# Performance work log

Hardware: AMD Instinct MI355X
Metric: run time of the kernel (lower is better)

Reference implementation:

```python
import jax, jax.numpy as jnp
import numpy as np

B, S, HID = 2, 1024, 4096
NH, NKV, HD = 32, 8, 128
EPS = 1e-6
ROPE_THETA = 1000000.0
SCALE = HD ** -0.5
NREP = NH // NKV


def _rope_tables(batch, seq, head_dim, theta):
    inv_freq = 1.0 / (theta ** (np.arange(0, head_dim, 2, dtype=np.float32) / head_dim))
    pos = np.arange(seq, dtype=np.float32)
    freqs = np.outer(pos, inv_freq)            # [S, HD/2]
    emb = np.concatenate([freqs, freqs], -1)   # [S, HD]
    cos = np.broadcast_to(np.cos(emb), (batch, seq, head_dim))
    sin = np.broadcast_to(np.sin(emb), (batch, seq, head_dim))
    return jnp.asarray(cos), jnp.asarray(sin)


def setup_inputs() -> dict:
    key = jax.random.key(0)
    k1, k2, k3 = jax.random.split(key, 3)
    hidden_states = jax.random.normal(k1, (B, S, HID), dtype=jnp.float32)
    cos, sin = _rope_tables(B, S, HD, ROPE_THETA)
    attention_mask = jnp.ones((B, 1, S, S), dtype=bool)
    w_qkv = jax.random.normal(k2, ((NH + 2 * NKV) * HD, HID), dtype=jnp.float32) * (HID ** -0.5)
    w_q_norm = jnp.ones((HD,), dtype=jnp.float32)
    w_k_norm = jnp.ones((HD,), dtype=jnp.float32)
    w_o = jax.random.normal(k3, (HID, NH * HD), dtype=jnp.float32) * ((NH * HD) ** -0.5)
    return {"hidden_states": hidden_states, "cos": cos, "sin": sin,
            "attention_mask": attention_mask, "w_qkv": w_qkv,
            "w_q_norm": w_q_norm, "w_k_norm": w_k_norm, "w_o": w_o}


def _rms_norm(x, w):
    var = jnp.mean(jnp.square(x), axis=-1, keepdims=True)
    return x * jax.lax.rsqrt(var + EPS) * w


def _rotate_half(x):
    x1, x2 = jnp.split(x, 2, axis=-1)
    return jnp.concatenate([-x2, x1], axis=-1)


def reference(hidden_states, cos, sin, attention_mask, w_qkv, w_q_norm, w_k_norm, w_o):
    qkv = jnp.einsum('bsh,oh->bso', hidden_states, w_qkv)  # [B,S,(NH+2NKV)*HD]
    q, k, v = jnp.split(qkv, [NH * HD, (NH + NKV) * HD], axis=-1)
    q = _rms_norm(q.reshape(B, S, NH, HD), w_q_norm).transpose(0, 2, 1, 3)   # [B,NH,S,HD]
    k = _rms_norm(k.reshape(B, S, NKV, HD), w_k_norm).transpose(0, 2, 1, 3)  # [B,NKV,S,HD]
    v = v.reshape(B, S, NKV, HD).transpose(0, 2, 1, 3)                        # [B,NKV,S,HD]
    c = cos[:, None, :, :]
    s = sin[:, None, :, :]
    q = q * c + _rotate_half(q) * s
    k = k * c + _rotate_half(k) * s
    k = jnp.repeat(k, NREP, axis=1)  # GQA repeat -> [B,NH,S,HD]
    v = jnp.repeat(v, NREP, axis=1)
    scores = jnp.einsum('bhqd,bhkd->bhqk', q, k) * SCALE
    scores = jnp.where(attention_mask, scores, jnp.finfo(scores.dtype).min)
    attn = jax.nn.softmax(scores, axis=-1)
    out = jnp.einsum('bhqk,bhkd->bhqd', attn, v)
    out = out.transpose(0, 2, 1, 3).reshape(B, S, NH * HD)
    return jnp.einsum('bsd,od->bso', out, w_o)
```

## Files before the change

kernel.cpp:

```cpp
#include <hip/hip_runtime.h>
#include <hip/hip_bf16.h>

typedef __bf16 bf16_t;
typedef bf16_t bf16x2 __attribute__((ext_vector_type(2)));
typedef bf16_t bf16x4 __attribute__((ext_vector_type(4)));
typedef bf16_t bf16x8 __attribute__((ext_vector_type(8)));
typedef float f32x4 __attribute__((ext_vector_type(4)));

#define DEVI __device__ __forceinline__

DEVI void gld_lds16(const void* g, void* l) {
  __builtin_amdgcn_global_load_lds(
      (const __attribute__((address_space(1))) void*)g,
      (__attribute__((address_space(3))) void*)l, 16, 0, 0);
}

__global__ __launch_bounds__(256) void cvt_f32_bf16(
    const float* __restrict__ in, bf16_t* __restrict__ out, long n) {
  long i = ((long)blockIdx.x * 256 + threadIdx.x) * 8;
  if (i >= n) return;
  float4 a = *(const float4*)(in + i);
  float4 b = *(const float4*)(in + i + 4);
  bf16x8 v = {(__bf16)a.x, (__bf16)a.y, (__bf16)a.z, (__bf16)a.w,
              (__bf16)b.x, (__bf16)b.y, (__bf16)b.z, (__bf16)b.w};
  *(bf16x8*)(out + i) = v;
}

__global__ __launch_bounds__(256) void cvt_f32_bf16_2(
    const float* __restrict__ ina, bf16_t* __restrict__ outa, long na,
    const float* __restrict__ inb, bf16_t* __restrict__ outb, long nb) {
  long i = ((long)blockIdx.x * 256 + threadIdx.x) * 8;
  const float* src;
  bf16_t* dst;
  if (i < na) {
    src = ina + i;
    dst = outa + i;
  } else {
    long j = i - na;
    if (j >= nb) return;
    src = inb + j;
    dst = outb + j;
  }
  float4 a = *(const float4*)src;
  float4 b = *(const float4*)(src + 4);
  bf16x8 v = {(__bf16)a.x, (__bf16)a.y, (__bf16)a.z, (__bf16)a.w,
              (__bf16)b.x, (__bf16)b.y, (__bf16)b.z, (__bf16)b.w};
  *(bf16x8*)dst = v;
}

template <int FC, int MINW, typename CT>
__global__ __launch_bounds__(512, MINW) void gemm128(
    const bf16_t* __restrict__ A, const bf16_t* __restrict__ W,
    CT* __restrict__ C, int M, int N, int K) {
  constexpr int BN = FC * 64;
  constexpr int P1 = FC / 2, P2 = FC - P1;
  __shared__ __align__(16) bf16_t As[2][128 * 64];
  __shared__ __align__(16) bf16_t Bs[2][BN * 64];
  const int tid = threadIdx.x, wave = tid >> 6, lane = tid & 63;
  const int q16 = lane & 15, gq = lane >> 4, sw = q16 & 7;
  const int wm = wave >> 2, wn = wave & 3;
  const int nM = M >> 7, nN = N / BN;
  const int cM = nM >> 1, cN = nN >> 2;
  const int xcd = (int)blockIdx.x & 7, wi = (int)blockIdx.x >> 3;
  const int tm = ((xcd >> 2) * cM + wi / cN) << 7;
  const int tn = ((xcd & 3) * cN + wi % cN) * BN;
  const int NT = K >> 6;
  const bf16_t* Ag = A + (size_t)tm * K;
  const bf16_t* Wg = W + (size_t)tn * K;
  const int sr = (wave << 3) + (lane >> 3);
  const int scol = (((lane & 7) ^ (sr & 7)) << 3);

#define STG(gbase, kq, uu, ldsbuf)                              \
  gld_lds16((gbase) + (size_t)((uu)*64 + sr) * K + (kq) + scol, \
            &(ldsbuf)[0] + (uu)*4096 + (wave << 9))

  f32x4 acc[4][FC];
#pragma unroll
  for (int i = 0; i < 4; ++i)
#pragma unroll
    for (int j = 0; j < FC; ++j) acc[i][j] = f32x4{0.f, 0.f, 0.f, 0.f};

  STG(Ag, 0, 0, As[0]);
  STG(Ag, 0, 1, As[0]);
#pragma unroll
  for (int u = 0; u < FC; ++u) STG(Wg, 0, u, Bs[0]);
  STG(Ag, 64, 0, As[1]);
  STG(Ag, 64, 1, As[1]);
  asm volatile("s_waitcnt vmcnt(2)" ::: "memory");
  __builtin_amdgcn_s_barrier();

  for (int t = 0; t < NT; ++t) {
    const int cur = t & 1;
    const bf16_t* Acur = As[cur];
    const bf16_t* Bcur = Bs[cur];
    const int k1 = (t + 1) << 6, k2 = (t + 2) << 6;
    bf16x8 afr[4][2];

#pragma unroll
    for (int fr = 0; fr < 4; ++fr) {
      const bf16_t* rp = Acur + (wm * 64 + fr * 16 + q16) * 64;
      afr[fr][0] = *(const bf16x8*)(rp + ((gq ^ sw) << 3));
      afr[fr][1] = *(const bf16x8*)(rp + (((4 + gq) ^ sw) << 3));
    }
    bf16x8 b1[P1][2];
#pragma unroll
    for (int fc = 0; fc < P1; ++fc) {
      const bf16_t* rp = Bcur + (wn * (16 * FC) + fc * 16 + q16) * 64;
      b1[fc][0] = *(const bf16x8*)(rp + ((gq ^ sw) << 3));
      b1[fc][1] = *(const bf16x8*)(rp + (((4 + gq) ^ sw) << 3));
    }
    if (t + 1 < NT) {
#pragma unroll
      for (int u = 0; u < FC; ++u) STG(Wg, k1, u, Bs[cur ^ 1]);
    }
    __builtin_amdgcn_s_barrier();
    __builtin_amdgcn_s_setprio(1);
#pragma unroll
    for (int fr = 0; fr < 4; ++fr)
#pragma unroll
      for (int fc = 0; fc < P1; ++fc)
#pragma unroll
        for (int kk = 0; kk < 2; ++kk)
          acc[fr][fc] = __builtin_amdgcn_mfma_f32_16x16x32_bf16(
              afr[fr][kk], b1[fc][kk], acc[fr][fc], 0, 0, 0);
    __builtin_amdgcn_s_setprio(0);
    asm volatile("" ::: "memory");
    __builtin_amdgcn_s_barrier();

    bf16x8 b2[P2][2];
#pragma unroll
    for (int f2 = 0; f2 < P2; ++f2) {
      const bf16_t* rp = Bcur + (wn * (16 * FC) + (P1 + f2) * 16 + q16) * 64;
      b2[f2][0] = *(const bf16x8*)(rp + ((gq ^ sw) << 3));
      b2[f2][1] = *(const bf16x8*)(rp + (((4 + gq) ^ sw) << 3));
    }
    if (t + 2 < NT) {
      STG(Ag, k2, 0, As[cur]);
      STG(Ag, k2, 1, As[cur]);
    }
    __builtin_amdgcn_s_barrier();
    __builtin_amdgcn_s_setprio(1);
#pragma unroll
    for (int fr = 0; fr < 4; ++fr)
#pragma unroll
      for (int f2 = 0; f2 < P2; ++f2)
#pragma unroll
        for (int kk = 0; kk < 2; ++kk)
          acc[fr][P1 + f2] = __builtin_amdgcn_mfma_f32_16x16x32_bf16(
              afr[fr][kk], b2[f2][kk], acc[fr][P1 + f2], 0, 0, 0);
    __builtin_amdgcn_s_setprio(0);
    if (t + 2 < NT)
      asm volatile("s_waitcnt vmcnt(2)" ::: "memory");
    else
      asm volatile("s_waitcnt vmcnt(0)" ::: "memory");
    __builtin_amdgcn_s_barrier();
  }

#pragma unroll
  for (int fr = 0; fr < 4; ++fr)
#pragma unroll
    for (int fc = 0; fc < FC; ++fc)
#pragma unroll
      for (int i = 0; i < 4; ++i) {
        int row = tm + wm * 64 + fr * 16 + gq * 4 + i;
        int col = tn + wn * (16 * FC) + fc * 16 + q16;
        C[(size_t)row * N + col] = (CT)acc[fr][fc][i];
      }
#undef STG
}

__global__ __launch_bounds__(256) void rope_scatter(
    const bf16_t* __restrict__ qkv, const float* __restrict__ cosb,
    const float* __restrict__ sinb, const float* __restrict__ wq,
    const float* __restrict__ wk, bf16_t* __restrict__ qb,
    bf16_t* __restrict__ kb, bf16_t* __restrict__ vt) {
  const int row = blockIdx.x;
  const int b = row >> 10, s = row & 1023;
  const int wave = threadIdx.x >> 6, lane = threadIdx.x & 63;
  const int d0 = 2 * lane;
  const float c0 = cosb[(size_t)row * 128 + d0];
  const float c1 = cosb[(size_t)row * 128 + d0 + 1];
  const float s0 = sinb[(size_t)row * 128 + d0];
  const float s1 = sinb[(size_t)row * 128 + d0 + 1];
  const float g0q = wq[d0], g1q = wq[d0 + 1];
  const float g0k = wk[d0], g1k = wk[d0 + 1];
  const float sign = (lane < 32) ? -1.f : 1.f;

  for (int h = wave; h < 32; h += 4) {
    const bf16_t* x = qkv + (size_t)row * 6144 + h * 128 + d0;
    float x0 = (float)x[0], x1 = (float)x[1];
    float ss = x0 * x0 + x1 * x1;
#pragma unroll
    for (int off = 1; off < 64; off <<= 1) ss += __shfl_xor(ss, off);
    float r = rsqrtf(ss * (1.0f / 128.0f) + 1e-6f);
    float n0 = x0 * r * g0q, n1 = x1 * r * g1q;
    float o0 = __shfl_xor(n0, 32), o1 = __shfl_xor(n1, 32);
    float y0 = n0 * c0 + sign * o0 * s0;
    float y1 = n1 * c1 + sign * o1 * s1;
    bf16_t* dst = qb + ((size_t)(b * 32 + h) * 1024 + s) * 128 + d0;
    dst[0] = (__bf16)y0;
    dst[1] = (__bf16)y1;
  }
  for (int h = wave; h < 8; h += 4) {
    const bf16_t* x = qkv + (size_t)row * 6144 + 4096 + h * 128 + d0;
    float x0 = (float)x[0], x1 = (float)x[1];
    float ss = x0 * x0 + x1 * x1;
#pragma unroll
    for (int off = 1; off < 64; off <<= 1) ss += __shfl_xor(ss, off);
    float r = rsqrtf(ss * (1.0f / 128.0f) + 1e-6f);
    float n0 = x0 * r * g0k, n1 = x1 * r * g1k;
    float o0 = __shfl_xor(n0, 32), o1 = __shfl_xor(n1, 32);
    float y0 = n0 * c0 + sign * o0 * s0;
    float y1 = n1 * c1 + sign * o1 * s1;
    bf16_t* dst = kb + ((size_t)(b * 8 + h) * 1024 + s) * 128 + d0;
    dst[0] = (__bf16)y0;
    dst[1] = (__bf16)y1;
  }
  for (int h = wave; h < 8; h += 4) {
    const bf16_t* x = qkv + (size_t)row * 6144 + 5120 + h * 128 + d0;
    bf16_t* dst = vt + ((size_t)(b * 8 + h) * 128 + d0) * 1024 + s;
    dst[0] = x[0];
    dst[1024] = x[1];
  }
}

__global__ __launch_bounds__(256, 2) void attn_fwd(
    const bf16_t* __restrict__ Qb, const bf16_t* __restrict__ Kb,
    const bf16_t* __restrict__ Vt, bf16_t* __restrict__ Ob) {
  __shared__ __align__(16) bf16_t Kl[2][64 * 128];
  __shared__ __align__(16) bf16_t Vl[2][128 * 64];
  __shared__ __align__(16) bf16_t Pl[4][32 * 64];
  const int tid = threadIdx.x, wave = tid >> 6, lane = tid & 63;
  const int q16 = lane & 15, g = lane >> 4;
  const int bid = blockIdx.x;
  const int bh = bid >> 3, qt = bid & 7;
  const int b = bh >> 5, h = bh & 31;
  const int kvh = (b << 3) + (h >> 2);
  const bf16_t* qp = Qb + ((size_t)bh * 1024 + qt * 128 + wave * 32) * 128;
  const bf16_t* kp = Kb + (size_t)kvh * (1024 * 128);
  const bf16_t* vp = Vt + (size_t)kvh * (128 * 1024);
  const float SCALE = 0.088388347648318447f;
  const float RESC_THR = 8.0f;
  const int sw = q16 & 7;

  bf16x8 qf[2][4];
#pragma unroll
  for (int m = 0; m < 2; ++m)
#pragma unroll
    for (int kc = 0; kc < 4; ++kc)
      qf[m][kc] = *(const bf16x8*)(qp + (m * 16 + q16) * 128 + kc * 32 + g * 8);

  f32x4 oacc[2][8];
#pragma unroll
  for (int m = 0; m < 2; ++m)
#pragma unroll
    for (int dc = 0; dc < 8; ++dc) oacc[m][dc] = f32x4{0.f, 0.f, 0.f, 0.f};
  float m_run[2] = {-3.0e38f, -3.0e38f}, l_run[2] = {0.f, 0.f};

#define STAGE_KV(buf, jj)                                                      \
  {                                                                            \
    _Pragma("unroll") for (int i = 0; i < 4; ++i) {                            \
      int n = (wave * 4 + i) * 64 + lane;                                      \
      int rk = n >> 4, ck = (n & 15) ^ (rk & 7);                               \
      gld_lds16(kp + (size_t)((jj) + rk) * 128 + ck * 8,                       \
                &Kl[buf][0] + (wave * 4 + i) * 512);                           \
      int rv = n >> 3, cv = (n & 7) ^ (rv & 7);                                \
      gld_lds16(vp + (size_t)rv * 1024 + (jj) + cv * 8,                        \
                &Vl[buf][0] + (wave * 4 + i) * 512);                           \
    }                                                                          \
  }

  STAGE_KV(0, 0);
  __syncthreads();
  int cur = 0;

  for (int jt = 0; jt < 16; ++jt) {
    if (jt < 15) STAGE_KV(cur ^ 1, (jt + 1) * 64);

    const bf16_t* Kc = &Kl[cur][0];
    const bf16_t* Vc = &Vl[cur][0];
    bf16_t* Plw = &Pl[wave][0];

    f32x4 st[2][4];
#pragma unroll
    for (int m = 0; m < 2; ++m)
#pragma unroll
      for (int t = 0; t < 4; ++t) st[m][t] = f32x4{0.f, 0.f, 0.f, 0.f};
#pragma unroll
    for (int t = 0; t < 4; ++t) {
      bf16x8 kf[4];
#pragma unroll
      for (int kc = 0; kc < 4; ++kc)
        kf[kc] = *(const bf16x8*)(Kc + (t * 16 + q16) * 128 + (((kc * 4 + g) ^ sw) << 3));
      __builtin_amdgcn_s_setprio(1);
#pragma unroll
      for (int m = 0; m < 2; ++m)
#pragma unroll
        for (int kc = 0; kc < 4; ++kc)
          st[m][t] = __builtin_amdgcn_mfma_f32_16x16x32_bf16(kf[kc], qf[m][kc], st[m][t], 0, 0, 0);
      __builtin_amdgcn_s_setprio(0);
    }

#pragma unroll
    for (int m = 0; m < 2; ++m) {
      float mxt = -3.0e38f;
#pragma unroll
      for (int t = 0; t < 4; ++t)
#pragma unroll
        for (int i = 0; i < 4; ++i) {
          float s = st[m][t][i] * SCALE;
          st[m][t][i] = s;
          mxt = fmaxf(mxt, s);
        }
      mxt = fmaxf(mxt, __shfl_xor(mxt, 16));
      mxt = fmaxf(mxt, __shfl_xor(mxt, 32));
      const bool keep = __all(mxt - m_run[m] <= RESC_THR);
      const float mnew = keep ? m_run[m] : fmaxf(m_run[m], mxt);
      float lsum = 0.f;
      const int prow = m * 16 + q16;
#pragma unroll
      for (int t = 0; t < 4; ++t) {
        float p0 = __expf(st[m][t][0] - mnew);
        float p1 = __expf(st[m][t][1] - mnew);
        float p2 = __expf(st[m][t][2] - mnew);
        float p3 = __expf(st[m][t][3] - mnew);
        lsum += (p0 + p1) + (p2 + p3);
        int k0 = t * 16 + g * 4;
        int a0 = prow * 64 + ((((k0 >> 3)) ^ sw) << 3) + (k0 & 7);
        *(bf16x4*)(Plw + a0) = bf16x4{(__bf16)p0, (__bf16)p1, (__bf16)p2, (__bf16)p3};
      }
      lsum += __shfl_xor(lsum, 16);
      lsum += __shfl_xor(lsum, 32);
      if (keep) {
        l_run[m] += lsum;
      } else {
        float alpha = __expf(m_run[m] - mnew);
        l_run[m] = l_run[m] * alpha + lsum;
        m_run[m] = mnew;
        float ar[4];
#pragma unroll
        for (int i = 0; i < 4; ++i) ar[i] = __shfl(alpha, g * 4 + i);
#pragma unroll
        for (int dc = 0; dc < 8; ++dc)
#pragma unroll
          for (int i = 0; i < 4; ++i) oacc[m][dc][i] *= ar[i];
      }
    }

#pragma unroll
    for (int ks = 0; ks < 2; ++ks) {
      bf16x8 pf0 = *(const bf16x8*)(Plw + (q16)*64 + (((ks * 4 + g) ^ sw) << 3));
      bf16x8 pf1 = *(const bf16x8*)(Plw + (16 + q16) * 64 + (((ks * 4 + g) ^ sw) << 3));
      __builtin_amdgcn_s_setprio(1);
#pragma unroll
      for (int dc = 0; dc < 8; ++dc) {
        bf16x8 vf = *(const bf16x8*)(Vc + (dc * 16 + q16) * 64 + (((ks * 4 + g) ^ sw) << 3));
        oacc[0][dc] = __builtin_amdgcn_mfma_f32_16x16x32_bf16(pf0, vf, oacc[0][dc], 0, 0, 0);
        oacc[1][dc] = __builtin_amdgcn_mfma_f32_16x16x32_bf16(pf1, vf, oacc[1][dc], 0, 0, 0);
      }
      __builtin_amdgcn_s_setprio(0);
    }

    __syncthreads();
    cur ^= 1;
  }

  const int rowbase = (b << 10) + qt * 128 + wave * 32;
#pragma unroll
  for (int m = 0; m < 2; ++m) {
    float lr[4];
#pragma unroll
    for (int i = 0; i < 4; ++i) lr[i] = __shfl(l_run[m], g * 4 + i);
#pragma unroll
    for (int dc = 0; dc < 8; ++dc)
#pragma unroll
      for (int i = 0; i < 4; ++i) {
        int row = rowbase + m * 16 + g * 4 + i;
        int col = (h << 7) + dc * 16 + q16;
        Ob[(size_t)row * 4096 + col] = (__bf16)(oacc[m][dc][i] / lr[i]);
      }
  }
#undef STAGE_KV
}

extern "C" void kernel_launch(void* const* d_in, const int* in_sizes, int n_in,
                              void* d_out, int out_size, void* d_ws,
                              size_t ws_size, hipStream_t stream) {
  const float* hidden = (const float*)d_in[0];
  const float* cosb = (const float*)d_in[1];
  const float* sinb = (const float*)d_in[2];
  const float* w_qkv = (const float*)d_in[4];
  const float* w_qn = (const float*)d_in[5];
  const float* w_kn = (const float*)d_in[6];
  const float* w_o = (const float*)d_in[7];
  float* out = (float*)d_out;

  char* ws = (char*)d_ws;
  bf16_t* wqkvb = (bf16_t*)ws;
  bf16_t* wob = (bf16_t*)ws;
  bf16_t* qb = (bf16_t*)(ws + 33554432);
  bf16_t* hb = (bf16_t*)(ws + 50331648);
  bf16_t* attno = hb;
  bf16_t* qkv = (bf16_t*)(ws + 67108864);
  bf16_t* kb = (bf16_t*)(ws + 92274688);
  bf16_t* vt = (bf16_t*)(ws + 96468992);

  cvt_f32_bf16_2<<<dim3(16384), dim3(256), 0, stream>>>(
      hidden, hb, 8388608, w_qkv, wqkvb, 25165824);
  gemm128<3, 4, bf16_t><<<dim3(512), dim3(512), 0, stream>>>(hb, wqkvb, qkv, 2048, 6144, 4096);
  cvt_f32_bf16<<<dim3(8192), dim3(256), 0, stream>>>(w_o, wob, 16777216);
  rope_scatter<<<dim3(2048), dim3(256), 0, stream>>>(qkv, cosb, sinb, w_qn, w_kn, qb, kb, vt);
  attn_fwd<<<dim3(64 * 8), dim3(256), 0, stream>>>(qb, kb, vt, attno);
  gemm128<2, 4, float><<<dim3(512), dim3(512), 0, stream>>>(attno, wob, out, 2048, 4096, 4096);
}
```

Baseline: 278.5 us.

## Split attention block into 8 waves of 16 query rows each

The attention kernel now runs 512 threads per block, with each of 8 waves owning 16 query rows instead of 4 waves owning 32. Per-wave register state (Q fragments, output accumulators, scores) is halved, and the K/V staging work is spread over twice as many waves. This is meant to raise wave-level parallelism and latency hiding on the same block count. In exchange, each K/V fragment read from LDS now feeds only one MFMA instead of two, which increases LDS traffic per FLOP.

```diff
diff --git a/kernel.cpp b/kernel.cpp
--- a/kernel.cpp
+++ b/kernel.cpp
@@ -224,49 +224,45 @@
   }
 }
 
-__global__ __launch_bounds__(256, 2) void attn_fwd(
+__global__ __launch_bounds__(512, 4) void attn_fwd(
     const bf16_t* __restrict__ Qb, const bf16_t* __restrict__ Kb,
     const bf16_t* __restrict__ Vt, bf16_t* __restrict__ Ob) {
   __shared__ __align__(16) bf16_t Kl[2][64 * 128];
   __shared__ __align__(16) bf16_t Vl[2][128 * 64];
-  __shared__ __align__(16) bf16_t Pl[4][32 * 64];
+  __shared__ __align__(16) bf16_t Pl[8][16 * 64];
   const int tid = threadIdx.x, wave = tid >> 6, lane = tid & 63;
   const int q16 = lane & 15, g = lane >> 4;
   const int bid = blockIdx.x;
   const int bh = bid >> 3, qt = bid & 7;
   const int b = bh >> 5, h = bh & 31;
   const int kvh = (b << 3) + (h >> 2);
-  const bf16_t* qp = Qb + ((size_t)bh * 1024 + qt * 128 + wave * 32) * 128;
+  const bf16_t* qp = Qb + ((size_t)bh * 1024 + qt * 128 + wave * 16) * 128;
   const bf16_t* kp = Kb + (size_t)kvh * (1024 * 128);
   const bf16_t* vp = Vt + (size_t)kvh * (128 * 1024);
   const float SCALE = 0.088388347648318447f;
   const float RESC_THR = 8.0f;
   const int sw = q16 & 7;
 
-  bf16x8 qf[2][4];
-#pragma unroll
-  for (int m = 0; m < 2; ++m)
-#pragma unroll
-    for (int kc = 0; kc < 4; ++kc)
-      qf[m][kc] = *(const bf16x8*)(qp + (m * 16 + q16) * 128 + kc * 32 + g * 8);
-
-  f32x4 oacc[2][8];
-#pragma unroll
-  for (int m = 0; m < 2; ++m)
-#pragma unroll
-    for (int dc = 0; dc < 8; ++dc) oacc[m][dc] = f32x4{0.f, 0.f, 0.f, 0.f};
-  float m_run[2] = {-3.0e38f, -3.0e38f}, l_run[2] = {0.f, 0.f};
+  bf16x8 qf[4];
+#pragma unroll
+  for (int kc = 0; kc < 4; ++kc)
+    qf[kc] = *(const bf16x8*)(qp + q16 * 128 + kc * 32 + g * 8);
+
+  f32x4 oacc[8];
+#pragma unroll
+  for (int dc = 0; dc < 8; ++dc) oacc[dc] = f32x4{0.f, 0.f, 0.f, 0.f};
+  float m_run = -3.0e38f, l_run = 0.f;
 
 #define STAGE_KV(buf, jj)                                                      \
   {                                                                            \
-    _Pragma("unroll") for (int i = 0; i < 4; ++i) {                            \
-      int n = (wave * 4 + i) * 64 + lane;                                      \
+    _Pragma("unroll") for (int i = 0; i < 2; ++i) {                            \
+      int n = (wave * 2 + i) * 64 + lane;                                      \
       int rk = n >> 4, ck = (n & 15) ^ (rk & 7);                               \
       gld_lds16(kp + (size_t)((jj) + rk) * 128 + ck * 8,                       \
-                &Kl[buf][0] + (wave * 4 + i) * 512);                           \
+                &Kl[buf][0] + (wave * 2 + i) * 512);                           \
       int rv = n >> 3, cv = (n & 7) ^ (rv & 7);                                \
       gld_lds16(vp + (size_t)rv * 1024 + (jj) + cv * 8,                        \
-                &Vl[buf][0] + (wave * 4 + i) * 512);                           \
+                &Vl[buf][0] + (wave * 2 + i) * 512);                           \
     }                                                                          \
   }
 
@@ -281,11 +277,9 @@
     const bf16_t* Vc = &Vl[cur][0];
     bf16_t* Plw = &Pl[wave][0];
 
-    f32x4 st[2][4];
-#pragma unroll
-    for (int m = 0; m < 2; ++m)
-#pragma unroll
-      for (int t = 0; t < 4; ++t) st[m][t] = f32x4{0.f, 0.f, 0.f, 0.f};
+    f32x4 st[4];
+#pragma unroll
+    for (int t = 0; t < 4; ++t) st[t] = f32x4{0.f, 0.f, 0.f, 0.f};
 #pragma unroll
     for (int t = 0; t < 4; ++t) {
       bf16x8 kf[4];
@@ -294,69 +288,63 @@
         kf[kc] = *(const bf16x8*)(Kc + (t * 16 + q16) * 128 + (((kc * 4 + g) ^ sw) << 3));
       __builtin_amdgcn_s_setprio(1);
 #pragma unroll
-      for (int m = 0; m < 2; ++m)
-#pragma unroll
-        for (int kc = 0; kc < 4; ++kc)
-          st[m][t] = __builtin_amdgcn_mfma_f32_16x16x32_bf16(kf[kc], qf[m][kc], st[m][t], 0, 0, 0);
+      for (int kc = 0; kc < 4; ++kc)
+        st[t] = __builtin_amdgcn_mfma_f32_16x16x32_bf16(kf[kc], qf[kc], st[t], 0, 0, 0);
       __builtin_amdgcn_s_setprio(0);
     }
 
-#pragma unroll
-    for (int m = 0; m < 2; ++m) {
+    {
       float mxt = -3.0e38f;
 #pragma unroll
       for (int t = 0; t < 4; ++t)
 #pragma unroll
         for (int i = 0; i < 4; ++i) {
-          float s = st[m][t][i] * SCALE;
-          st[m][t][i] = s;
+          float s = st[t][i] * SCALE;
+          st[t][i] = s;
           mxt = fmaxf(mxt, s);
         }
       mxt = fmaxf(mxt, __shfl_xor(mxt, 16));
       mxt = fmaxf(mxt, __shfl_xor(mxt, 32));
-      const bool keep = __all(mxt - m_run[m] <= RESC_THR);
-      const float mnew = keep ? m_run[m] : fmaxf(m_run[m], mxt);
+      const bool keep = __all(mxt - m_run <= RESC_THR);
+      const float mnew = keep ? m_run : fmaxf(m_run, mxt);
       float lsum = 0.f;
-      const int prow = m * 16 + q16;
 #pragma unroll
       for (int t = 0; t < 4; ++t) {
-        float p0 = __expf(st[m][t][0] - mnew);
-        float p1 = __expf(st[m][t][1] - mnew);
-        float p2 = __expf(st[m][t][2] - mnew);
-        float p3 = __expf(st[m][t][3] - mnew);
+        float p0 = __expf(st[t][0] - mnew);
+        float p1 = __expf(st[t][1] - mnew);
+        float p2 = __expf(st[t][2] - mnew);
+        float p3 = __expf(st[t][3] - mnew);
         lsum += (p0 + p1) + (p2 + p3);
         int k0 = t * 16 + g * 4;
-        int a0 = prow * 64 + ((((k0 >> 3)) ^ sw) << 3) + (k0 & 7);
+        int a0 = q16 * 64 + ((((k0 >> 3)) ^ sw) << 3) + (k0 & 7);
         *(bf16x4*)(Plw + a0) = bf16x4{(__bf16)p0, (__bf16)p1, (__bf16)p2, (__bf16)p3};
       }
       lsum += __shfl_xor(lsum, 16);
       lsum += __shfl_xor(lsum, 32);
       if (keep) {
-        l_run[m] += lsum;
+        l_run += lsum;
       } else {
-        float alpha = __expf(m_run[m] - mnew);
-        l_run[m] = l_run[m] * alpha + lsum;
-        m_run[m] = mnew;
+        float alpha = __expf(m_run - mnew);
+        l_run = l_run * alpha + lsum;
+        m_run = mnew;
         float ar[4];
 #pragma unroll
         for (int i = 0; i < 4; ++i) ar[i] = __shfl(alpha, g * 4 + i);
 #pragma unroll
         for (int dc = 0; dc < 8; ++dc)
 #pragma unroll
-          for (int i = 0; i < 4; ++i) oacc[m][dc][i] *= ar[i];
+          for (int i = 0; i < 4; ++i) oacc[dc][i] *= ar[i];
       }
     }
 
 #pragma unroll
     for (int ks = 0; ks < 2; ++ks) {
-      bf16x8 pf0 = *(const bf16x8*)(Plw + (q16)*64 + (((ks * 4 + g) ^ sw) << 3));
-      bf16x8 pf1 = *(const bf16x8*)(Plw + (16 + q16) * 64 + (((ks * 4 + g) ^ sw) << 3));
+      bf16x8 pf = *(const bf16x8*)(Plw + q16 * 64 + (((ks * 4 + g) ^ sw) << 3));
       __builtin_amdgcn_s_setprio(1);
 #pragma unroll
       for (int dc = 0; dc < 8; ++dc) {
         bf16x8 vf = *(const bf16x8*)(Vc + (dc * 16 + q16) * 64 + (((ks * 4 + g) ^ sw) << 3));
-        oacc[0][dc] = __builtin_amdgcn_mfma_f32_16x16x32_bf16(pf0, vf, oacc[0][dc], 0, 0, 0);
-        oacc[1][dc] = __builtin_amdgcn_mfma_f32_16x16x32_bf16(pf1, vf, oacc[1][dc], 0, 0, 0);
+        oacc[dc] = __builtin_amdgcn_mfma_f32_16x16x32_bf16(pf, vf, oacc[dc], 0, 0, 0);
       }
       __builtin_amdgcn_s_setprio(0);
     }
@@ -365,21 +353,18 @@
     cur ^= 1;
   }
 
-  const int rowbase = (b << 10) + qt * 128 + wave * 32;
-#pragma unroll
-  for (int m = 0; m < 2; ++m) {
-    float lr[4];
-#pragma unroll
-    for (int i = 0; i < 4; ++i) lr[i] = __shfl(l_run[m], g * 4 + i);
-#pragma unroll
-    for (int dc = 0; dc < 8; ++dc)
-#pragma unroll
-      for (int i = 0; i < 4; ++i) {
-        int row = rowbase + m * 16 + g * 4 + i;
-        int col = (h << 7) + dc * 16 + q16;
-        Ob[(size_t)row * 4096 + col] = (__bf16)(oacc[m][dc][i] / lr[i]);
-      }
-  }
+  const int rowbase = (b << 10) + qt * 128 + wave * 16;
+  float lr[4];
+#pragma unroll
+  for (int i = 0; i < 4; ++i) lr[i] = __shfl(l_run, g * 4 + i);
+#pragma unroll
+  for (int dc = 0; dc < 8; ++dc)
+#pragma unroll
+    for (int i = 0; i < 4; ++i) {
+      int row = rowbase + g * 4 + i;
+      int col = (h << 7) + dc * 16 + q16;
+      Ob[(size_t)row * 4096 + col] = (__bf16)(oacc[dc][i] / lr[i]);
+    }
 #undef STAGE_KV
 }
 
@@ -410,6 +395,6 @@
   gemm128<3, 4, bf16_t><<<dim3(512), dim3(512), 0, stream>>>(hb, wqkvb, qkv, 2048, 6144, 4096);
   cvt_f32_bf16<<<dim3(8192), dim3(256), 0, stream>>>(w_o, wob, 16777216);
   rope_scatter<<<dim3(2048), dim3(256), 0, stream>>>(qkv, cosb, sinb, w_qn, w_kn, qb, kb, vt);
-  attn_fwd<<<dim3(64 * 8), dim3(256), 0, stream>>>(qb, kb, vt, attno);
+  attn_fwd<<<dim3(64 * 8), dim3(512), 0, stream>>>(qb, kb, vt, attno);
   gemm128<2, 4, float><<<dim3(512), dim3(512), 0, stream>>>(attno, wob, out, 2048, 4096, 4096);
 }
```

Measured after the change: 275.8 us. About the same (-1.0%).
